# Performance work log

Hardware: AMD Instinct MI355X
Metric: run time of the kernel (lower is better)

Reference implementation:

```python
import jax, jax.numpy as jnp
import numpy as np

# Module config: RoDAlignMax(aligned_height=9, aligned_width=9, spatial_scale=0.25)
# Internally RoDAlignFunction is called with aligned_height+1, aligned_width+1,
# then max_pool2d(kernel=2, stride=1) shrinks each spatial dim by 1.
AH, AW = 10, 10          # pre-pool sampling grid (aligned_{h,w} + 1)
SPATIAL_SCALE = 0.25


def _rod_align(features, rois, ah, aw, scale):
    """RoDAlign: uniform bilinear sampling grid over the WHOLE feature map,
    with samples falling INSIDE the ROI zeroed out (region-of-discard).
    features: [B,C,H,W], rois: [R,5]=(batch_ind,x1,y1,x2,y2) -> [R,C,ah,aw]."""
    B, C, H, W = features.shape
    dt = features.dtype
    bidx = rois[:, 0].astype(jnp.int32)                              # [R]
    x1 = rois[:, 1] * scale
    y1 = rois[:, 2] * scale
    x2 = rois[:, 3] * scale
    y2 = rois[:, 4] * scale
    # uniform grid spanning the full feature map
    h = jnp.arange(ah, dtype=dt) * ((H - 1.0) / (ah - 1.0))          # [AH]
    w = jnp.arange(aw, dtype=dt) * ((W - 1.0) / (aw - 1.0))          # [AW]
    h0 = jnp.minimum(jnp.floor(h), H - 2).astype(jnp.int32)
    w0 = jnp.minimum(jnp.floor(w), W - 2).astype(jnp.int32)
    hr = (h - h0.astype(dt))[:, None, None]                          # [AH,1,1]
    wr = (w - w0.astype(dt))[None, :, None]                          # [1,AW,1]
    b = bidx[:, None, None]                                          # [R,1,1]
    hi0 = h0[None, :, None]; hi1 = hi0 + 1                           # [1,AH,1]
    wi0 = w0[None, None, :]; wi1 = wi0 + 1                           # [1,1,AW]
    # four corner gathers; advanced idx dims go first -> [R,AH,AW,C]
    ul = features[b, :, hi0, wi0]
    ur = features[b, :, hi0, wi1]
    dl = features[b, :, hi1, wi0]
    dr = features[b, :, hi1, wi1]
    out = (ul * (1 - hr) * (1 - wr) + ur * (1 - hr) * wr
           + dl * hr * (1 - wr) + dr * hr * wr)                      # [R,AH,AW,C]
    # zero samples inside the ROI (the kept crop region is discarded)
    in_h = (h[None, :] >= y1[:, None]) & (h[None, :] <= y2[:, None])  # [R,AH]
    in_w = (w[None, :] >= x1[:, None]) & (w[None, :] <= x2[:, None])  # [R,AW]
    inside = in_h[:, :, None] & in_w[:, None, :]                      # [R,AH,AW]
    out = jnp.where(inside[..., None], jnp.zeros((), dt), out)
    return jnp.transpose(out, (0, 3, 1, 2))                           # [R,C,AH,AW]


def _maxpool2x2_s1(x):
    # max_pool2d(kernel_size=2, stride=1) on [..., H, W]
    return jnp.maximum(jnp.maximum(x[..., :-1, :-1], x[..., :-1, 1:]),
                       jnp.maximum(x[..., 1:, :-1], x[..., 1:, 1:]))


def setup_inputs() -> dict:
    key = jax.random.key(0)
    k1, k2, k3, k4, k5 = jax.random.split(key, 5)
    B, C, H, W = 4, 256, 64, 64
    R = 2048
    img = H / SPATIAL_SCALE  # 256.0, input-image coordinate extent
    features = jax.random.normal(k1, (B, C, H, W), dtype=jnp.float32)
    bidx = jax.random.randint(k2, (R,), 0, B).astype(jnp.float32)
    x1 = jax.random.uniform(k3, (R,), dtype=jnp.float32) * (img * 0.5)
    y1 = jax.random.uniform(k4, (R,), dtype=jnp.float32) * (img * 0.5)
    wh = jax.random.uniform(k5, (R, 2), dtype=jnp.float32) * (img * 0.45) + img * 0.05
    x2 = jnp.minimum(x1 + wh[:, 0], img - 1.0)
    y2 = jnp.minimum(y1 + wh[:, 1], img - 1.0)
    rois = jnp.stack([bidx, x1, y1, x2, y2], axis=1)  # [R,5]
    return {"features": features, "rois": rois}


def reference(features, rois):
    x = _rod_align(features, rois, AH, AW, SPATIAL_SCALE)  # [R,C,10,10]
    return _maxpool2x2_s1(x)                               # [R,C,9,9]
```

## Files before the change

### kernel.cpp

```cpp
#include <hip/hip_runtime.h>


#define NR 2048

typedef float f4 __attribute__((ext_vector_type(4)));

__global__ __launch_bounds__(256) void rod_table(const float* __restrict__ F,
                                                 f4* __restrict__ T) {
    int idx = blockIdx.x * 256 + threadIdx.x;
    if (idx < 82944) {
        unsigned bc = ((unsigned)idx * 25891u) >> 21;
        int q = idx - 81 * (int)bc;
        int i = (q * 57) >> 9;
        int j = q - 9 * i;
        const float* fp = F + ((int)bc << 12) + i * 448 + j * 7;
        float v00 = fp[0], v01 = fp[7], v10 = fp[448], v11 = fp[455];
        f4 t;
        t.x = fmaxf(v00, v01);
        t.y = fmaxf(v10, v11);
        t.z = fmaxf(v00, v10);
        t.w = fmaxf(v01, v11);
        T[idx] = t;
    }
}

__global__ __launch_bounds__(256) void rod_main4(const f4* __restrict__ T,
                                                 const float* __restrict__ rois,
                                                 float* __restrict__ out) {
    const int tid = threadIdx.x;
    const int r   = blockIdx.x;

    const float x1 = rois[r * 5 + 1] * 0.25f;
    const float y1 = rois[r * 5 + 2] * 0.25f;
    const float x2 = rois[r * 5 + 3] * 0.25f;
    const float y2 = rois[r * 5 + 4] * 0.25f;
    const int   b  = (int)rois[r * 5 + 0];

    unsigned inh = 0u, inw = 0u;
    #pragma unroll
    for (int t = 0; t < 10; ++t) {
        float s = 7.0f * (float)t;
        if ((s >= y1) && (s <= y2)) inh |= (1u << t);
        if ((s >= x1) && (s <= x2)) inw |= (1u << t);
    }

    const f4* Tb  = T + b * 20736;
    float*    dst = out + (size_t)r * 20736;

    unsigned c0 = ((unsigned)tid * 25891u) >> 21;
    int q  = tid - 81 * (int)c0;
    int el = tid;

    #pragma unroll 3
    for (int k = 0; k < 81; ++k) {
        f4 t = Tb[el];
        int i = (q * 57) >> 9;
        int j = q - 9 * i;
        unsigned hb = (inh >> i) & 3u;
        unsigned wb = (inw >> j) & 3u;

        float rowA = (hb == 1u) ? t.y : ((hb == 2u) ? t.x : 0.0f);
        float colA = (wb == 1u) ? t.w : ((wb == 2u) ? t.z : 0.0f);
        float inMax  = fmaxf(fmaxf(rowA, colA), 0.0f);
        float outMax = fmaxf(t.x, t.y);
        bool  anyIn  = (hb != 0u) && (wb != 0u);

        __builtin_nontemporal_store(anyIn ? inMax : outMax, dst + el);

        el += 256;
        q += 13; q = (q >= 81) ? q - 81 : q;
    }
}

extern "C" void kernel_launch(void* const* d_in, const int* in_sizes, int n_in,
                              void* d_out, int out_size, void* d_ws, size_t ws_size,
                              hipStream_t stream) {
    const float* F    = (const float*)d_in[0];
    const float* rois = (const float*)d_in[1];
    float*       out  = (float*)d_out;
    f4*          T    = (f4*)d_ws;

    rod_table<<<dim3(324), dim3(256), 0, stream>>>(F, T);
    rod_main4<<<dim3(NR), dim3(256), 0, stream>>>(T, rois, out);
}
```

Before: 187.6 us.

## Split pooled table into scalar max table plus sparse fix-up reads

The table kernel now writes a compact scalar table holding the plain 2x2 max alongside the four-way partial-max table. The main kernel reads the scalar table with vectorized f4 loads and stores, and fetches the f4 partial maxima only for positions where the ROI mask requires a fix-up, using a shared LUT built per ROI. This cuts the main loop's read traffic by about four times for uncovered positions. The f4 table is parked in the tail of the output buffer, so the last 16 ROIs are handled by a separate kernel that recomputes fix-ups directly from the features. That adds a third launch and depends on kernel ordering to avoid overwriting the table before it is read.

After: 233.4 us. 24.4% more time.

```diff
diff --git a/kernel.cpp b/kernel.cpp
--- a/kernel.cpp
+++ b/kernel.cpp
@@ -1,12 +1,15 @@
 #include <hip/hip_runtime.h>
 
 
-#define NR 2048
-
 typedef float f4 __attribute__((ext_vector_type(4)));
 
-__global__ __launch_bounds__(256) void rod_table(const float* __restrict__ F,
-                                                 f4* __restrict__ T) {
+#define NQ 81
+#define NPR 20736
+#define TAIL_BASE 2032
+
+__global__ __launch_bounds__(256) void rod_tables(const float* __restrict__ F,
+                                                  float* __restrict__ M4,
+                                                  f4* __restrict__ T16) {
     int idx = blockIdx.x * 256 + threadIdx.x;
     if (idx < 82944) {
         unsigned bc = ((unsigned)idx * 25891u) >> 21;
@@ -20,55 +23,137 @@
         t.y = fmaxf(v10, v11);
         t.z = fmaxf(v00, v10);
         t.w = fmaxf(v01, v11);
-        T[idx] = t;
+        T16[idx] = t;
+        M4[idx] = fmaxf(t.x, t.y);
     }
 }
 
-__global__ __launch_bounds__(256) void rod_main4(const f4* __restrict__ T,
-                                                 const float* __restrict__ rois,
-                                                 float* __restrict__ out) {
-    const int tid = threadIdx.x;
-    const int r   = blockIdx.x;
-
-    const float x1 = rois[r * 5 + 1] * 0.25f;
-    const float y1 = rois[r * 5 + 2] * 0.25f;
-    const float x2 = rois[r * 5 + 3] * 0.25f;
-    const float y2 = rois[r * 5 + 4] * 0.25f;
-    const int   b  = (int)rois[r * 5 + 0];
-
-    unsigned inh = 0u, inw = 0u;
+__device__ __forceinline__ void roi_masks(const float* __restrict__ rois, int r,
+                                          unsigned& inh, unsigned& inw, int& b) {
+    float x1 = rois[r * 5 + 1] * 0.25f, y1 = rois[r * 5 + 2] * 0.25f;
+    float x2 = rois[r * 5 + 3] * 0.25f, y2 = rois[r * 5 + 4] * 0.25f;
+    b = (int)rois[r * 5 + 0];
+    inh = 0u; inw = 0u;
     #pragma unroll
     for (int t = 0; t < 10; ++t) {
         float s = 7.0f * (float)t;
-        if ((s >= y1) && (s <= y2)) inh |= (1u << t);
-        if ((s >= x1) && (s <= x2)) inw |= (1u << t);
+        if (s >= y1 && s <= y2) inh |= 1u << t;
+        if (s >= x1 && s <= x2) inw |= 1u << t;
     }
+}
 
-    const f4* Tb  = T + b * 20736;
-    float*    dst = out + (size_t)r * 20736;
+__device__ __forceinline__ void build_lut(unsigned* lut, int tid,
+                                          unsigned inh, unsigned inw) {
+    if (tid < NQ) {
+        int i = (tid * 57) >> 9;
+        int j = tid - 9 * i;
+        unsigned hb = (inh >> i) & 3u, wb = (inw >> j) & 3u;
+        lut[tid] = (hb && wb) ? ((hb << 2) | wb) : 0u;
+    }
+}
 
-    unsigned c0 = ((unsigned)tid * 25891u) >> 21;
-    int q  = tid - 81 * (int)c0;
-    int el = tid;
+__device__ __forceinline__ float fix_from_t(f4 t, unsigned sel) {
+    unsigned hb = sel >> 2, wb = sel & 3u;
+    float rowA = (hb == 1u) ? t.y : ((hb == 2u) ? t.x : 0.0f);
+    float colA = (wb == 1u) ? t.w : ((wb == 2u) ? t.z : 0.0f);
+    return fmaxf(fmaxf(rowA, colA), 0.0f);
+}
 
-    #pragma unroll 3
-    for (int k = 0; k < 81; ++k) {
-        f4 t = Tb[el];
-        int i = (q * 57) >> 9;
-        int j = q - 9 * i;
-        unsigned hb = (inh >> i) & 3u;
-        unsigned wb = (inw >> j) & 3u;
+__global__ __launch_bounds__(256, 8) void rod_main5(const float* __restrict__ M4,
+                                                    const f4* __restrict__ T16,
+                                                    const float* __restrict__ rois,
+                                                    float* __restrict__ out) {
+    __shared__ unsigned lut[NQ];
+    const int tid = threadIdx.x;
+    const int r = blockIdx.x;
+    unsigned inh, inw; int b;
+    roi_masks(rois, r, inh, inw, b);
+    build_lut(lut, tid, inh, inw);
+    __syncthreads();
 
-        float rowA = (hb == 1u) ? t.y : ((hb == 2u) ? t.x : 0.0f);
-        float colA = (wb == 1u) ? t.w : ((wb == 2u) ? t.z : 0.0f);
-        float inMax  = fmaxf(fmaxf(rowA, colA), 0.0f);
-        float outMax = fmaxf(t.x, t.y);
-        bool  anyIn  = (hb != 0u) && (wb != 0u);
+    const float* Mb = M4 + b * NPR;
+    const f4*    Tb = T16 + b * NPR;
+    float*       dst = out + (size_t)r * NPR;
 
-        __builtin_nontemporal_store(anyIn ? inMax : outMax, dst + el);
+    int e  = tid * 4;
+    int q0 = e - 81 * (int)(((unsigned)e * 25891u) >> 21);
 
-        el += 256;
-        q += 13; q = (q >= 81) ? q - 81 : q;
+    #pragma unroll 4
+    for (int k = 0; k < 20; ++k) {
+        f4 m = *(const f4*)(Mb + e);
+        float res[4];
+        #pragma unroll
+        for (int ii = 0; ii < 4; ++ii) {
+            int qi = q0 + ii; qi = (qi >= NQ) ? qi - NQ : qi;
+            unsigned sel = lut[qi];
+            float v = m[ii];
+            if (sel) v = fix_from_t(Tb[e + ii], sel);
+            res[ii] = v;
+        }
+        *(f4*)(dst + e) = (f4){res[0], res[1], res[2], res[3]};
+        e += 1024;
+        q0 += 52; q0 = (q0 >= NQ) ? q0 - NQ : q0;
+    }
+    if (tid < 64) {
+        f4 m = *(const f4*)(Mb + e);
+        float res[4];
+        #pragma unroll
+        for (int ii = 0; ii < 4; ++ii) {
+            int qi = q0 + ii; qi = (qi >= NQ) ? qi - NQ : qi;
+            unsigned sel = lut[qi];
+            float v = m[ii];
+            if (sel) v = fix_from_t(Tb[e + ii], sel);
+            res[ii] = v;
+        }
+        *(f4*)(dst + e) = (f4){res[0], res[1], res[2], res[3]};
+    }
+}
+
+__global__ __launch_bounds__(256) void rod_tail(const float* __restrict__ M4,
+                                                const float* __restrict__ F,
+                                                const float* __restrict__ rois,
+                                                float* __restrict__ out) {
+    __shared__ unsigned lut[NQ];
+    const int tid = threadIdx.x;
+    const int r = TAIL_BASE + blockIdx.x;
+    unsigned inh, inw; int b;
+    roi_masks(rois, r, inh, inw, b);
+    build_lut(lut, tid, inh, inw);
+    __syncthreads();
+
+    const float* Mb = M4 + b * NPR;
+    const float* Fb = F + ((size_t)b << 20);
+    float*       dst = out + (size_t)r * NPR;
+
+    int e  = tid * 4;
+    int q0 = e - 81 * (int)(((unsigned)e * 25891u) >> 21);
+
+    for (int k = 0; k < 21; ++k) {
+        if (e < NPR) {
+            f4 m = *(const f4*)(Mb + e);
+            float res[4];
+            #pragma unroll
+            for (int ii = 0; ii < 4; ++ii) {
+                int qi = q0 + ii; qi = (qi >= NQ) ? qi - NQ : qi;
+                unsigned sel = lut[qi];
+                float v = m[ii];
+                if (sel) {
+                    int c = (int)(((unsigned)(e + ii) * 25891u) >> 21);
+                    int i = (qi * 57) >> 9;
+                    int j = qi - 9 * i;
+                    const float* fp = Fb + (c << 12) + i * 448 + j * 7;
+                    float v00 = fp[0], v01 = fp[7], v10 = fp[448], v11 = fp[455];
+                    f4 t;
+                    t.x = fmaxf(v00, v01); t.y = fmaxf(v10, v11);
+                    t.z = fmaxf(v00, v10); t.w = fmaxf(v01, v11);
+                    v = fix_from_t(t, sel);
+                }
+                res[ii] = v;
+            }
+            *(f4*)(dst + e) = (f4){res[0], res[1], res[2], res[3]};
+        }
+        e += 1024;
+        q0 += 52; q0 = (q0 >= NQ) ? q0 - NQ : q0;
     }
 }
 
@@ -78,8 +163,10 @@
     const float* F    = (const float*)d_in[0];
     const float* rois = (const float*)d_in[1];
     float*       out  = (float*)d_out;
-    f4*          T    = (f4*)d_ws;
+    float*       M4   = (float*)d_ws;
+    f4*          T16  = (f4*)(out + (size_t)TAIL_BASE * NPR);
 
-    rod_table<<<dim3(324), dim3(256), 0, stream>>>(F, T);
-    rod_main4<<<dim3(NR), dim3(256), 0, stream>>>(T, rois, out);
+    rod_tables<<<dim3(324),  dim3(256), 0, stream>>>(F, M4, T16);
+    rod_main5 <<<dim3(2032), dim3(256), 0, stream>>>(M4, T16, rois, out);
+    rod_tail  <<<dim3(16),   dim3(256), 0, stream>>>(M4, F, rois, out);
 }
```
